# Kernel optimization log

Hardware: AMD Instinct MI355X
Metric: run time of the kernel (lower is better)

The kernel has to match this reference:

```python
import jax, jax.numpy as jnp
import numpy as np

N_HEAD = 16


def setup_inputs() -> dict:
    key = jax.random.key(0)
    ks = jax.random.split(key, 5)
    B, T, C = 2, 2048, 1024
    s = 1.0 / np.sqrt(C)
    inp = {
        "x": jax.random.normal(ks[0], (B, T, C), dtype=jnp.float32),
        "Wq": jax.random.normal(ks[1], (C, C), dtype=jnp.float32) * s,
        "bq": jnp.zeros((C,), dtype=jnp.float32),
        "Wk": jax.random.normal(ks[2], (C, C), dtype=jnp.float32) * s,
        "bk": jnp.zeros((C,), dtype=jnp.float32),
        "Wv": jax.random.normal(ks[3], (C, C), dtype=jnp.float32) * s,
        "bv": jnp.zeros((C,), dtype=jnp.float32),
        "Wp": jax.random.normal(ks[4], (C, C), dtype=jnp.float32) * s,
        "bp": jnp.zeros((C,), dtype=jnp.float32),
    }
    return inp


def reference(x, Wq, bq, Wk, bk, Wv, bv, Wp, bp):
    B, T, C = x.shape
    H = N_HEAD
    D = C // H
    # linear projections (torch Linear: x @ W.T + b)
    q = (x @ Wq.T + bq).reshape(B, T, H, D)
    k = (x @ Wk.T + bk).reshape(B, T, H, D)
    v = (x @ Wv.T + bv).reshape(B, T, H, D)
    # scaled dot-product attention (NO causal mask in original forward)
    att = jnp.einsum("bthd,bshd->bhts", q, k) * (1.0 / np.sqrt(D))
    att = jax.nn.softmax(att, axis=-1)
    y = jnp.einsum("bhts,bshd->bthd", att, v).reshape(B, T, C)
    # output projection (dropouts are identity at p=0 / eval)
    return y @ Wp.T + bp
```

## Files before the change

### kernel.cpp

```cpp
#include <hip/hip_runtime.h>
#include <hip/hip_bf16.h>

typedef __attribute__((ext_vector_type(4))) float f32x4;
typedef __attribute__((ext_vector_type(16))) float f32x16;
typedef __attribute__((ext_vector_type(8))) short bf16x8;
typedef __attribute__((ext_vector_type(2))) unsigned int u32x2;

#define T_SEQ 2048
#define C_DIM 1024
#define NH 16
#define DHD 64

__device__ __forceinline__ unsigned cvtpk_bf16(float lo, float hi) {
    unsigned r;
    asm("v_cvt_pk_bf16_f32 %0, %1, %2" : "=v"(r) : "v"(lo), "v"(hi));
    return r;
}

__device__ __forceinline__ void async_copy16(void* lds, const void* g) {
    __builtin_amdgcn_global_load_lds(
        (const __attribute__((address_space(1))) unsigned int*)(uintptr_t)g,
        (__attribute__((address_space(3))) unsigned int*)(unsigned int)(uintptr_t)lds,
        16, 0, 0);
}

__global__ __launch_bounds__(256) void cvt_all(const float* __restrict__ x,
                                               const float* __restrict__ Wq, const float* __restrict__ Wk,
                                               const float* __restrict__ Wv, const float* __restrict__ Wp,
                                               __hip_bfloat16* __restrict__ xb,
                                               __hip_bfloat16* __restrict__ wf,
                                               __hip_bfloat16* __restrict__ wpb) {
    int i = blockIdx.x * blockDim.x + threadIdx.x;
    const float* src; __hip_bfloat16* dst; int off;
    if (i < 1048576) { src = x; dst = xb; off = i; }
    else {
        int j = i - 1048576; int wi = j >> 18; off = j & 262143;
        switch (wi) {
            case 0:  src = Wq; dst = wf;           break;
            case 1:  src = Wk; dst = wf + 1048576; break;
            case 2:  src = Wv; dst = wf + 2097152; break;
            default: src = Wp; dst = wpb;          break;
        }
    }
    float4 v = *(const float4*)(src + (size_t)off * 4);
    size_t o = (size_t)off * 4;
    dst[o + 0] = __float2bfloat16(v.x);
    dst[o + 1] = __float2bfloat16(v.y);
    dst[o + 2] = __float2bfloat16(v.z);
    dst[o + 3] = __float2bfloat16(v.w);
}

__global__ __launch_bounds__(512) void gemm_qkv(const __hip_bfloat16* __restrict__ A,
                                                const __hip_bfloat16* __restrict__ Bw,
                                                const float* __restrict__ biasq,
                                                const float* __restrict__ biask,
                                                const float* __restrict__ biasv,
                                                __hip_bfloat16* __restrict__ oq,
                                                __hip_bfloat16* __restrict__ okk,
                                                __hip_bfloat16* __restrict__ ovt) {
    __shared__ __align__(16) char lds[131072];

    const int wg = ((int)blockIdx.x & 7) * 24 + ((int)blockIdx.x >> 3);
    const int m0 = (wg & 15) * 256;
    const int n0 = (wg >> 4) * 256;

    const int tid = threadIdx.x;
    const int w = tid >> 6, l = tid & 63;
    const int wr = w >> 2, wc = w & 3;
    const int lg = l >> 4, lr = l & 15;

    const int sr0 = tid >> 3;
    const int sc0 = (tid & 7) * 16;
    const int gc0 = sc0 ^ ((sr0 & 7) << 4);
    const size_t goff = (size_t)sr0 * 2048 + gc0;

    const char* Ag = (const char*)A + (size_t)m0 * 2048;
    const char* Bg = (const char*)Bw + (size_t)n0 * 2048;

    auto STAGE_A = [&](int buf, int half, int kt) {
        const char* g = Ag + (size_t)(half * 128) * 2048 + kt * 128 + goff;
        char* d = lds + (buf * 2 + half) * 16384 + w * 1024;
        async_copy16(d, g);
        async_copy16(d + 8192, g + (size_t)64 * 2048);
    };
    auto STAGE_B = [&](int buf, int half, int kt) {
        const char* g = Bg + (size_t)(half * 128) * 2048 + kt * 128 + goff;
        char* d = lds + 65536 + (buf * 2 + half) * 16384 + w * 1024;
        async_copy16(d, g);
        async_copy16(d + 8192, g + (size_t)64 * 2048);
    };

    const int sw = (lr & 7) << 4;
    auto LDA = [&](bf16x8* af, int buf, int mq) {
        const char* base = lds + (buf * 2 + wr) * 16384;
        #pragma unroll
        for (int m = 0; m < 4; m++) {
            const int r = (mq * 4 + m) * 16 + lr;
            #pragma unroll
            for (int kk = 0; kk < 2; kk++)
                af[m * 2 + kk] = *(const bf16x8*)(base + r * 128 + ((kk * 64 + lg * 16) ^ sw));
        }
    };
    auto LDB = [&](bf16x8* bfv, int buf, int nq) {
        const char* base = lds + 65536 + (buf * 2 + (wc >> 1)) * 16384;
        #pragma unroll
        for (int n = 0; n < 2; n++) {
            const int r = (wc & 1) * 64 + (nq * 2 + n) * 16 + lr;
            #pragma unroll
            for (int kk = 0; kk < 2; kk++)
                bfv[n * 2 + kk] = *(const bf16x8*)(base + r * 128 + ((kk * 64 + lg * 16) ^ sw));
        }
    };

    f32x4 acc[8][4] = {};
    auto MF = [&](const bf16x8* af, const bf16x8* bfv, int mq, int nq) {
        #pragma unroll
        for (int m = 0; m < 4; m++)
            #pragma unroll
            for (int n = 0; n < 2; n++)
                #pragma unroll
                for (int kk = 0; kk < 2; kk++)
                    acc[mq * 4 + m][nq * 2 + n] = __builtin_amdgcn_mfma_f32_16x16x32_bf16(
                        af[m * 2 + kk], bfv[n * 2 + kk], acc[mq * 4 + m][nq * 2 + n], 0, 0, 0);
    };

#define PH_OPEN()  __builtin_amdgcn_sched_barrier(0); \
                   __builtin_amdgcn_s_barrier(); \
                   asm volatile("s_waitcnt lgkmcnt(0)" ::: "memory"); \
                   __builtin_amdgcn_sched_barrier(0); \
                   __builtin_amdgcn_s_setprio(1);
#define PH_CLOSE() __builtin_amdgcn_s_setprio(0); \
                   __builtin_amdgcn_sched_barrier(0); \
                   __builtin_amdgcn_s_barrier();
#define PH_CLOSE_VM() __builtin_amdgcn_s_setprio(0); \
                   asm volatile("s_waitcnt vmcnt(6)" ::: "memory"); \
                   __builtin_amdgcn_sched_barrier(0); \
                   __builtin_amdgcn_s_barrier();

    bf16x8 af[8], bf0[4], bf1[4];

    STAGE_B(0, 0, 0); STAGE_B(0, 1, 0); STAGE_A(0, 0, 0); STAGE_A(0, 1, 0);
    STAGE_B(1, 0, 1); STAGE_B(1, 1, 1); STAGE_A(1, 0, 1);
    asm volatile("s_waitcnt vmcnt(6)" ::: "memory");
    __builtin_amdgcn_sched_barrier(0);
    __builtin_amdgcn_s_barrier();

    for (int it = 0; it < 8; ++it) {
        const int t1 = 2 * it + 1;
        const int c2 = (2 * it + 2 < 16) ? 2 * it + 2 : 14;
        const int c3 = (2 * it + 3 < 16) ? 2 * it + 3 : 15;
        const int b2 = c2 & 1, b3 = c3 & 1;

        LDA(af, 0, 0); LDB(bf0, 0, 0);
        STAGE_A(1, 1, t1);
        PH_OPEN(); MF(af, bf0, 0, 0); PH_CLOSE();
        LDB(bf1, 0, 1);
        PH_OPEN(); MF(af, bf1, 0, 1); PH_CLOSE();
        LDA(af, 0, 1);
        STAGE_B(b2, 0, c2);
        PH_OPEN(); MF(af, bf1, 1, 1); PH_CLOSE();
        STAGE_B(b2, 1, c2); STAGE_A(b2, 0, c2);
        PH_OPEN(); MF(af, bf0, 1, 0); PH_CLOSE_VM();

        LDA(af, 1, 0); LDB(bf0, 1, 0);
        STAGE_A(b2, 1, c2);
        PH_OPEN(); MF(af, bf0, 0, 0); PH_CLOSE();
        LDB(bf1, 1, 1);
        PH_OPEN(); MF(af, bf1, 0, 1); PH_CLOSE();
        LDA(af, 1, 1);
        STAGE_B(b3, 0, c3);
        PH_OPEN(); MF(af, bf1, 1, 1); PH_CLOSE();
        STAGE_B(b3, 1, c3); STAGE_A(b3, 0, c3);
        PH_OPEN(); MF(af, bf0, 1, 0); PH_CLOSE_VM();
    }
#undef PH_OPEN
#undef PH_CLOSE
#undef PH_CLOSE_VM

    const int proj = n0 >> 10;
    const float* bias = (proj == 0) ? biasq : (proj == 1) ? biask : biasv;
    const float bsc = (proj == 0) ? 0.125f : 1.0f;
    #pragma unroll
    for (int m = 0; m < 8; m++)
        #pragma unroll
        for (int n = 0; n < 4; n++)
            #pragma unroll
            for (int rr = 0; rr < 4; rr++) {
                int row = m0 + wr * 128 + m * 16 + lg * 4 + rr;
                int col = n0 + wc * 64 + n * 16 + lr;
                int colL = col & (C_DIM - 1);
                float val = (acc[m][n][rr] + bias[colL]) * bsc;
                int b = row >> 11, t = row & 2047, hh = colL >> 6, dd = colL & 63;
                if (proj < 2) {
                    __hip_bfloat16* dst = (proj == 0) ? oq : okk;
                    dst[(((size_t)(b * NH + hh)) * T_SEQ + t) * DHD + dd] = __float2bfloat16(val);
                } else {
                    ovt[(((size_t)(b * NH + hh)) * DHD + dd) * T_SEQ + t] = __float2bfloat16(val);
                }
            }
}

__global__ __launch_bounds__(256) void gemm_proj(const __hip_bfloat16* __restrict__ A,
                                                 const __hip_bfloat16* __restrict__ Bw,
                                                 const float* __restrict__ biasp,
                                                 float* __restrict__ outf) {
    __shared__ __align__(16) char As[128 * 128];
    __shared__ __align__(16) char Bs[128 * 128];

    const int nwg = gridDim.x;
    const int cpx = nwg >> 3;
    const int wg = ((int)blockIdx.x & 7) * cpx + ((int)blockIdx.x >> 3);
    const int m0 = (wg & 31) * 128;
    const int n0 = (wg >> 5) * 128;

    const int tid = threadIdx.x;
    const int w = tid >> 6, l = tid & 63;
    const int wr = w >> 1, wc = w & 1;
    const int lg = l >> 4, lr = l & 15;

    const char* Ag = (const char*)A + (size_t)m0 * 2048;
    const char* Bg = (const char*)Bw + (size_t)n0 * 2048;
    const int lrow = l >> 3;
    const int scol = (l & 7) * 16;

    f32x4 acc[4][4] = {};

    for (int kt = 0; kt < 16; ++kt) {
        __syncthreads();
        #pragma unroll
        for (int i = 0; i < 4; i++) {
            const int rb = w * 32 + i * 8;
            const size_t go = (size_t)(rb + lrow) * 2048 + (size_t)kt * 128 + scol;
            async_copy16(&As[rb * 128], Ag + go);
            async_copy16(&Bs[rb * 128], Bg + go);
        }
        __syncthreads();
        #pragma unroll
        for (int kk = 0; kk < 2; kk++) {
            bf16x8 af[4], bfr[4];
            #pragma unroll
            for (int m = 0; m < 4; m++)
                af[m] = *(const bf16x8*)(&As[(wr * 64 + m * 16 + lr) * 128 + kk * 64 + lg * 16]);
            #pragma unroll
            for (int n = 0; n < 4; n++)
                bfr[n] = *(const bf16x8*)(&Bs[(wc * 64 + n * 16 + lr) * 128 + kk * 64 + lg * 16]);
            #pragma unroll
            for (int m = 0; m < 4; m++)
                #pragma unroll
                for (int n = 0; n < 4; n++)
                    acc[m][n] = __builtin_amdgcn_mfma_f32_16x16x32_bf16(af[m], bfr[n], acc[m][n], 0, 0, 0);
        }
    }

    #pragma unroll
    for (int m = 0; m < 4; m++)
        #pragma unroll
        for (int n = 0; n < 4; n++)
            #pragma unroll
            for (int r = 0; r < 4; r++) {
                int row = m0 + wr * 64 + m * 16 + lg * 4 + r;
                int col = n0 + wc * 64 + n * 16 + lr;
                outf[(size_t)row * C_DIM + col] = acc[m][n][r] + biasp[col];
            }
}

__global__ __launch_bounds__(256) void attn3(const __hip_bfloat16* __restrict__ Q,
                                             const __hip_bfloat16* __restrict__ K,
                                             const __hip_bfloat16* __restrict__ Vt,
                                             __hip_bfloat16* __restrict__ Y) {
    const int bid = blockIdx.x;
    const int xcd = bid & 7, slot = bid >> 3;
    const int head = xcd * 4 + (slot & 3);
    const int qblk = slot >> 2;

    const int tid = threadIdx.x;
    const int w = tid >> 6, l = tid & 63;
    const int lq = l & 31, hi = l >> 5;
    const int q0 = qblk * 128 + w * 32;

    __shared__ __align__(16) char Ks[3][8192];
    __shared__ __align__(16) char Vs[3][8192];
    __shared__ float bc[4][32];

    const char* Kb = (const char*)(K + (size_t)head * T_SEQ * DHD);
    const char* Vb = (const char*)(Vt + (size_t)head * DHD * T_SEQ);

    bf16x8 qf[4];
    {
        const char* qrow = (const char*)(Q + ((size_t)head * T_SEQ + q0 + lq) * DHD);
        #pragma unroll
        for (int t = 0; t < 4; t++) qf[t] = *(const bf16x8*)(qrow + t * 32 + hi * 16);
    }

    f32x16 yacc[2] = {};
    float ls0 = 0.f, ls1 = 0.f, ls2 = 0.f, ls3 = 0.f;

    const int o0 = (2 * w) * 1024 + l * 16;
    const int o1 = o0 + 1024;
    const int r0 = o0 >> 7, c0b = o0 & 127;
    const int r1 = o1 >> 7, c1b = o1 & 127;
    const int wads0 = r0 * 128 + (c0b ^ ((r0 & 7) << 4));
    const int wads1 = r1 * 128 + (c1b ^ ((r1 & 7) << 4));
    const char* vsrc0 = Vb + (size_t)r0 * (T_SEQ * 2) + c0b;
    const char* vsrc1 = Vb + (size_t)r1 * (T_SEQ * 2) + c1b;

    float4 kreg0, kreg1, vreg0, vreg1;
    auto stage_load = [&](int tile) {
        const char* kb2 = Kb + (size_t)tile * 8192;
        kreg0 = *(const float4*)(kb2 + o0);
        kreg1 = *(const float4*)(kb2 + o1);
        vreg0 = *(const float4*)(vsrc0 + (size_t)tile * 128);
        vreg1 = *(const float4*)(vsrc1 + (size_t)tile * 128);
    };
    auto stage_write = [&](int buf) {
        *(float4*)(&Ks[buf][wads0]) = kreg0;
        *(float4*)(&Ks[buf][wads1]) = kreg1;
        *(float4*)(&Vs[buf][wads0]) = vreg0;
        *(float4*)(&Vs[buf][wads1]) = vreg1;
    };

    auto qk = [&](int buf, f32x16& s0h, f32x16& s1h) {
        s0h = f32x16{}; s1h = f32x16{};
        const char* base0 = Ks[buf] + (0 * 32 + lq) * 128;
        const char* base1 = Ks[buf] + (1 * 32 + lq) * 128;
        const int sw0 = (lq & 7) << 4;
        #pragma unroll
        for (int t = 0; t < 4; t++) {
            bf16x8 kf0 = *(const bf16x8*)(base0 + ((t * 32 + hi * 16) ^ sw0));
            s0h = __builtin_amdgcn_mfma_f32_32x32x16_bf16(kf0, qf[t], s0h, 0, 0, 0);
        }
        #pragma unroll
        for (int t = 0; t < 4; t++) {
            bf16x8 kf1 = *(const bf16x8*)(base1 + ((t * 32 + hi * 16) ^ sw0));
            s1h = __builtin_amdgcn_mfma_f32_32x32x16_bf16(kf1, qf[t], s1h, 0, 0, 0);
        }
    };

    auto sm_exp = [&](f32x16& a, f32x16& b) {
        #pragma unroll
        for (int r = 0; r < 16; r += 4) {
            a[r + 0] = __expf(a[r + 0]); a[r + 1] = __expf(a[r + 1]);
            a[r + 2] = __expf(a[r + 2]); a[r + 3] = __expf(a[r + 3]);
            b[r + 0] = __expf(b[r + 0]); b[r + 1] = __expf(b[r + 1]);
            b[r + 2] = __expf(b[r + 2]); b[r + 3] = __expf(b[r + 3]);
            ls0 += a[r + 0] + b[r + 0];
            ls1 += a[r + 1] + b[r + 1];
            ls2 += a[r + 2] + b[r + 2];
            ls3 += a[r + 3] + b[r + 3];
        }
    };

    auto pv = [&](int buf, const f32x16& a, const f32x16& b) {
        unsigned pw0[8], pw1[8];
        #pragma unroll
        for (int M = 0; M < 4; M++) {
            const int u = M * 4;
            pw0[M] = cvtpk_bf16(a[u + 0], a[u + 1]);
            pw1[M] = cvtpk_bf16(a[u + 2], a[u + 3]);
            pw0[M + 4] = cvtpk_bf16(b[u + 0], b[u + 1]);
            pw1[M + 4] = cvtpk_bf16(b[u + 2], b[u + 3]);
        }
        #pragma unroll
        for (int t = 0; t < 4; t++) {
            u32x2 s0p = __builtin_amdgcn_permlane32_swap(pw0[2 * t], pw0[2 * t + 1], false, false);
            u32x2 s1p = __builtin_amdgcn_permlane32_swap(pw1[2 * t], pw1[2 * t + 1], false, false);
            union { unsigned u[4]; bf16x8 v; } af;
            af.u[0] = s0p.x; af.u[1] = s1p.x; af.u[2] = s0p.y; af.u[3] = s1p.y;
            #pragma unroll
            for (int dh = 0; dh < 2; dh++) {
                const int row = dh * 32 + lq;
                bf16x8 vf = *(const bf16x8*)(&Vs[buf][row * 128 + ((t * 32 + hi * 16) ^ ((row & 7) << 4))]);
                yacc[dh] = __builtin_amdgcn_mfma_f32_32x32x16_bf16(af.v, vf, yacc[dh], 0, 0, 0);
            }
        }
    };

    f32x16 sA0, sA1, sB0, sB1;
    stage_load(0); stage_write(0);
    stage_load(1); stage_write(1);
    stage_load(2);
    __syncthreads();
    qk(0, sA0, sA1);

    for (int t = 0; t < 32; t += 2) {
        qk((t + 1) % 3, sB0, sB1);
        if (t + 2 < 32) {
            stage_write((t + 2) % 3);
            if (t + 3 < 32) stage_load(t + 3);
        }
        sm_exp(sA0, sA1);
        pv(t % 3, sA0, sA1);
        __syncthreads();
        const int t1 = t + 1;
        if (t1 + 1 < 32) qk((t1 + 1) % 3, sA0, sA1);
        if (t1 + 2 < 32) {
            stage_write((t1 + 2) % 3);
            if (t1 + 3 < 32) stage_load(t1 + 3);
        }
        sm_exp(sB0, sB1);
        pv(t1 % 3, sB0, sB1);
        __syncthreads();
    }

    float lsum = (ls0 + ls1) + (ls2 + ls3);
    lsum += __shfl_xor(lsum, 32);
    float inv = 1.0f / lsum;
    if (hi == 0) bc[w][lq] = inv;
    asm volatile("s_waitcnt lgkmcnt(0)" ::: "memory");
    __builtin_amdgcn_sched_barrier(0);

    const int b = head >> 4, h16 = head & 15;
    const size_t rowbase = (size_t)b * T_SEQ + q0;
    #pragma unroll
    for (int r = 0; r < 16; r++) {
        const int crow = (r & 3) + 8 * (r >> 2) + 4 * hi;
        const float iv = bc[w][crow];
        const size_t row = rowbase + crow;
        Y[row * C_DIM + h16 * DHD + lq]      = __float2bfloat16(yacc[0][r] * iv);
        Y[row * C_DIM + h16 * DHD + 32 + lq] = __float2bfloat16(yacc[1][r] * iv);
    }
}

extern "C" void kernel_launch(void* const* d_in, const int* in_sizes, int n_in,
                              void* d_out, int out_size, void* d_ws, size_t ws_size,
                              hipStream_t stream) {
    (void)in_sizes; (void)n_in; (void)out_size; (void)ws_size;
    const float* x  = (const float*)d_in[0];
    const float* Wq = (const float*)d_in[1];
    const float* bq = (const float*)d_in[2];
    const float* Wk = (const float*)d_in[3];
    const float* bk = (const float*)d_in[4];
    const float* Wv = (const float*)d_in[5];
    const float* bv = (const float*)d_in[6];
    const float* Wp = (const float*)d_in[7];
    const float* bp = (const float*)d_in[8];
    float* out = (float*)d_out;

    char* ws = (char*)d_ws;
    const size_t MC = (size_t)4096 * C_DIM;
    const size_t CC = (size_t)C_DIM * C_DIM;
    __hip_bfloat16* xb  = (__hip_bfloat16*)ws;  ws += MC * 2;
    __hip_bfloat16* wf  = (__hip_bfloat16*)ws;  ws += 3 * CC * 2;
    __hip_bfloat16* wpb = (__hip_bfloat16*)ws;  ws += CC * 2;
    __hip_bfloat16* qb  = (__hip_bfloat16*)ws;  ws += MC * 2;
    __hip_bfloat16* kb  = (__hip_bfloat16*)ws;  ws += MC * 2;
    __hip_bfloat16* vtb = (__hip_bfloat16*)ws;  ws += MC * 2;
    __hip_bfloat16* yb  = (__hip_bfloat16*)ws;  ws += MC * 2;

    cvt_all<<<8192, 256, 0, stream>>>(x, Wq, Wk, Wv, Wp, xb, wf, wpb);

    gemm_qkv<<<192, 512, 0, stream>>>(xb, wf, bq, bk, bv, qb, kb, vtb);

    attn3<<<512, 256, 0, stream>>>(qb, kb, vtb, yb);

    gemm_proj<<<256, 256, 0, stream>>>(yb, wpb, bp, out);
}
```

Baseline: 140.4 us.

## Vectorize bf16 convert stores, remap QKV GEMM tiles per XCD, hand-tune attention barriers

The conversion kernel now packs four bf16 values into one 8-byte store instead of four scalar 2-byte stores. The QKV GEMM block-to-tile mapping now gives each XCD a 4x6 rectangle of output tiles, so blocks on the same L2 share A and B panels. The attention loop replaces __syncthreads with an explicit lgkmcnt wait, s_barrier and sched_barrier, and adds a vmcnt(0) wait before each LDS stage write. The explicit waits could serialize global loads more than the compiler would, and the sched_barrier limits instruction interleaving.

```diff
diff --git a/kernel.cpp b/kernel.cpp
--- a/kernel.cpp
+++ b/kernel.cpp
@@ -43,11 +43,11 @@
         }
     }
     float4 v = *(const float4*)(src + (size_t)off * 4);
-    size_t o = (size_t)off * 4;
-    dst[o + 0] = __float2bfloat16(v.x);
-    dst[o + 1] = __float2bfloat16(v.y);
-    dst[o + 2] = __float2bfloat16(v.z);
-    dst[o + 3] = __float2bfloat16(v.w);
+    __hip_bfloat16 h0 = __float2bfloat16(v.x), h1 = __float2bfloat16(v.y);
+    __hip_bfloat16 h2 = __float2bfloat16(v.z), h3 = __float2bfloat16(v.w);
+    union { __hip_bfloat16 h[4]; u32x2 u; } p;
+    p.h[0] = h0; p.h[1] = h1; p.h[2] = h2; p.h[3] = h3;
+    *(u32x2*)(dst + (size_t)off * 4) = p.u;
 }
 
 __global__ __launch_bounds__(512) void gemm_qkv(const __hip_bfloat16* __restrict__ A,
@@ -60,9 +60,10 @@
                                                 __hip_bfloat16* __restrict__ ovt) {
     __shared__ __align__(16) char lds[131072];
 
-    const int wg = ((int)blockIdx.x & 7) * 24 + ((int)blockIdx.x >> 3);
-    const int m0 = (wg & 15) * 256;
-    const int n0 = (wg >> 4) * 256;
+    const int xcd = (int)blockIdx.x & 7, loc = (int)blockIdx.x >> 3;
+    const int mloc = loc / 6, nloc = loc - mloc * 6;
+    const int m0 = ((xcd & 3) * 4 + mloc) * 256;
+    const int n0 = ((xcd >> 2) * 6 + nloc) * 256;
 
     const int tid = threadIdx.x;
     const int w = tid >> 6, l = tid & 63;
@@ -264,7 +265,7 @@
             }
 }
 
-__global__ __launch_bounds__(256) void attn3(const __hip_bfloat16* __restrict__ Q,
+__global__ __launch_bounds__(256) void attn4(const __hip_bfloat16* __restrict__ Q,
                                              const __hip_bfloat16* __restrict__ K,
                                              const __hip_bfloat16* __restrict__ Vt,
                                              __hip_bfloat16* __restrict__ Y) {
@@ -385,21 +386,27 @@
     for (int t = 0; t < 32; t += 2) {
         qk((t + 1) % 3, sB0, sB1);
         if (t + 2 < 32) {
+            asm volatile("s_waitcnt vmcnt(0)" ::: "memory");
             stage_write((t + 2) % 3);
             if (t + 3 < 32) stage_load(t + 3);
         }
         sm_exp(sA0, sA1);
         pv(t % 3, sA0, sA1);
-        __syncthreads();
+        asm volatile("s_waitcnt lgkmcnt(0)" ::: "memory");
+        __builtin_amdgcn_s_barrier();
+        __builtin_amdgcn_sched_barrier(0);
         const int t1 = t + 1;
         if (t1 + 1 < 32) qk((t1 + 1) % 3, sA0, sA1);
         if (t1 + 2 < 32) {
+            asm volatile("s_waitcnt vmcnt(0)" ::: "memory");
             stage_write((t1 + 2) % 3);
             if (t1 + 3 < 32) stage_load(t1 + 3);
         }
         sm_exp(sB0, sB1);
         pv(t1 % 3, sB0, sB1);
-        __syncthreads();
+        asm volatile("s_waitcnt lgkmcnt(0)" ::: "memory");
+        __builtin_amdgcn_s_barrier();
+        __builtin_amdgcn_sched_barrier(0);
     }
 
     float lsum = (ls0 + ls1) + (ls2 + ls3);
@@ -451,7 +458,7 @@
 
     gemm_qkv<<<192, 512, 0, stream>>>(xb, wf, bq, bk, bv, qb, kb, vtb);
 
-    attn3<<<512, 256, 0, stream>>>(qb, kb, vtb, yb);
+    attn4<<<512, 256, 0, stream>>>(qb, kb, vtb, yb);
 
     gemm_proj<<<256, 256, 0, stream>>>(yb, wpb, bp, out);
 }
```

Result: no change. 140.2 us (-0.1%).
